# Kernel optimization log

Hardware: AMD Instinct MI355X
Metric: run time of the kernel (lower is better)

## Reference

```python
import jax, jax.numpy as jnp
import numpy as np

B, S, H, E = 32, 2048, 512, 512

def setup_inputs() -> dict:
    key = jax.random.key(0)
    ks = jax.random.split(key, 7)
    data_alpha = jax.random.normal(ks[0], (B, S, H), dtype=jnp.float32)
    data_beta  = jax.random.normal(ks[1], (B, S, H), dtype=jnp.float32)
    data_embed = jax.random.normal(ks[2], (B, S, E), dtype=jnp.float32)
    # Linear params (PyTorch-style: y = x @ W.T + b), scaled ~1/sqrt(H)
    Wb = jax.random.normal(ks[3], (E, H), dtype=jnp.float32) * (1.0 / np.sqrt(H))
    bb = jnp.zeros((E,), dtype=jnp.float32)
    Wa = jax.random.normal(ks[4], (1, H), dtype=jnp.float32) * (1.0 / np.sqrt(H))
    ba = jnp.zeros((1,), dtype=jnp.float32)
    return {"data_alpha": data_alpha, "data_beta": data_beta, "data_embed": data_embed,
            "Wb": Wb, "bb": bb, "Wa": Wa, "ba": ba}

def reference(data_alpha, data_beta, data_embed, Wb, bb, Wa, ba):
    # beta_weights = tanh(Linear(data_beta)) : [B,S,E]
    beta = jnp.tanh(jnp.einsum('bsh,eh->bse', data_beta, Wb) + bb)
    # scalar correlate per timestep, exponentiated : [B,S]
    c = jnp.einsum('bsh,oh->bso', data_alpha, Wa)[..., 0] + ba[0]
    w = jnp.exp(c)
    # Original builds alpha[b,i,j] = w[b,j]*[j<=i] / (cumsum_j<=i w) and contracts
    # sum_j alpha[b,i,j]*beta[b,j,e]*embed[b,j,e]; equivalent O(S*E) cumsum form:
    v = beta * data_embed                               # [B,S,E]
    num = jnp.cumsum(w[:, :, None] * v, axis=1)         # [B,S,E]
    den = jnp.cumsum(w, axis=1)[:, :, None] + 1e-10     # [B,S,1]
    return num / den
```

## Files before the change

kernel.cpp:

```cpp
#include <hip/hip_runtime.h>
#include <math.h>

#define Bn 32
#define Sn 2048
#define Hn 512
#define En 512
#define Mn (Bn*Sn)
#define CH 128
#define NCH (Sn/CH)
#define BK 64

using short8  = __attribute__((ext_vector_type(8))) short;
using floatx4 = __attribute__((ext_vector_type(4))) float;

__device__ __forceinline__ unsigned short f2bf(float x) {
    unsigned u = __float_as_uint(x);
    u += 0x7FFFu + ((u >> 16) & 1u);
    return (unsigned short)(u >> 16);
}

__device__ __forceinline__ float fast_tanh(float x) {
    x = fminf(20.f, fmaxf(-20.f, x));
    float e = __expf(2.f * x);
    return (e - 1.f) * __builtin_amdgcn_rcpf(e + 1.f);
}

__device__ __forceinline__ void load_lds16(const unsigned short* g, unsigned short* l) {
    __builtin_amdgcn_global_load_lds((const __attribute__((address_space(1))) void*)g,
                                     (__attribute__((address_space(3))) void*)l,
                                     16, 0, 0);
}

__global__ __launch_bounds__(256) void k_conv(const float* __restrict__ in,
                                              unsigned short* __restrict__ out, int n8) {
    int i = blockIdx.x * 256 + threadIdx.x;
    if (i >= n8) return;
    const float4 a = ((const float4*)in)[2*i];
    const float4 b = ((const float4*)in)[2*i + 1];
    short8 o;
    o[0]=f2bf(a.x); o[1]=f2bf(a.y); o[2]=f2bf(a.z); o[3]=f2bf(a.w);
    o[4]=f2bf(b.x); o[5]=f2bf(b.y); o[6]=f2bf(b.z); o[7]=f2bf(b.w);
    ((short8*)out)[i] = o;
}

__global__ __launch_bounds__(256) void k_w(const float* __restrict__ alpha,
                                           const float* __restrict__ Wa,
                                           const float* __restrict__ ba,
                                           float* __restrict__ wout) {
    const int lane = threadIdx.x & 63;
    const int wq   = threadIdx.x >> 6;
    const int row  = blockIdx.x * 4 + wq;
    const float* ap = alpha + (size_t)row * Hn + lane * 8;
    const float* wp = Wa + lane * 8;
    float4 a0 = *(const float4*)ap;
    float4 a1 = *(const float4*)(ap + 4);
    float4 w0 = *(const float4*)wp;
    float4 w1 = *(const float4*)(wp + 4);
    float s = a0.x*w0.x + a0.y*w0.y + a0.z*w0.z + a0.w*w0.w
            + a1.x*w1.x + a1.y*w1.y + a1.z*w1.z + a1.w*w1.w;
    #pragma unroll
    for (int off = 32; off; off >>= 1) s += __shfl_down(s, off, 64);
    if (lane == 0) wout[row] = expf(s + ba[0]);
}

__global__ __launch_bounds__(64) void k_scan_w(const float* __restrict__ w,
                                               float* __restrict__ cw) {
    const int b = blockIdx.x;
    const int lane = threadIdx.x;
    const float* wp = w  + (size_t)b * Sn;
    float*       cp = cw + (size_t)b * Sn;
    float carry = 0.f;
    for (int c = 0; c < Sn; c += 64) {
        float v = wp[c + lane];
        #pragma unroll
        for (int off = 1; off < 64; off <<= 1) {
            float t = __shfl_up(v, off, 64);
            if (lane >= off) v += t;
        }
        float o = carry + v;
        cp[c + lane] = o;
        carry = __shfl(o, 63, 64);
    }
}

__global__ __launch_bounds__(256) void k_gemm2(const unsigned short* __restrict__ Abf,
                                               const unsigned short* __restrict__ Bbf,
                                               const float* __restrict__ bbias,
                                               const float* __restrict__ wv,
                                               const float* __restrict__ embed,
                                               float* __restrict__ outp,
                                               float* __restrict__ partial) {
    __shared__ unsigned short lds_a[128 * BK];
    __shared__ unsigned short lds_b[128 * BK];
    const int tid  = threadIdx.x;
    const int lane = tid & 63, wq = tid >> 6;
    const int wave_n = wq & 1, wave_m = wq >> 1;
    const int blockN = blockIdx.x * 128;
    const int blockM = blockIdx.y * 128;
    const int lrow = lane & 15;
    const int quad = lane >> 4;
    const int srow = wq * 32 + (lane >> 3);
    const int scol = (lane & 7) * 8;

    floatx4 acc[4][4];
    #pragma unroll
    for (int i = 0; i < 4; i++)
        #pragma unroll
        for (int j = 0; j < 4; j++) acc[i][j] = (floatx4){0.f, 0.f, 0.f, 0.f};

    const unsigned short* Ag = Abf + (size_t)(blockM + srow) * Hn + scol;
    const unsigned short* Bg = Bbf + (size_t)(blockN + srow) * Hn + scol;
    unsigned short* la = &lds_a[(wq * 32) * BK];
    unsigned short* lb = &lds_b[(wq * 32) * BK];

    for (int k0 = 0; k0 < Hn; k0 += BK) {
        #pragma unroll
        for (int it = 0; it < 4; it++) {
            load_lds16(Ag + (size_t)(it * 8) * Hn + k0, la + it * 8 * BK);
            load_lds16(Bg + (size_t)(it * 8) * Hn + k0, lb + it * 8 * BK);
        }
        __syncthreads();
        #pragma unroll
        for (int kk = 0; kk < BK; kk += 32) {
            short8 afr[4], bfr[4];
            #pragma unroll
            for (int j = 0; j < 4; j++)
                bfr[j] = *(const short8*)&lds_b[(wave_n*64 + j*16 + lrow)*BK + kk + quad*8];
            #pragma unroll
            for (int i = 0; i < 4; i++)
                afr[i] = *(const short8*)&lds_a[(wave_m*64 + i*16 + lrow)*BK + kk + quad*8];
            #pragma unroll
            for (int i = 0; i < 4; i++)
                #pragma unroll
                for (int j = 0; j < 4; j++)
                    acc[i][j] = __builtin_amdgcn_mfma_f32_16x16x32_bf16(afr[i], bfr[j], acc[i][j], 0, 0, 0);
        }
        __syncthreads();
    }

    float colsum[4] = {0.f, 0.f, 0.f, 0.f};
    #pragma unroll
    for (int j = 0; j < 4; j++) {
        const int c = blockN + wave_n * 64 + j * 16 + lrow;
        const float bbv = bbias[c];
        #pragma unroll
        for (int i = 0; i < 4; i++) {
            const int rbase = blockM + wave_m * 64 + i * 16 + quad * 4;
            #pragma unroll
            for (int reg = 0; reg < 4; reg++) {
                const int r = rbase + reg;
                const size_t idx = (size_t)r * En + c;
                const float t = wv[r] * fast_tanh(acc[i][j][reg] + bbv) * embed[idx];
                outp[idx] = t;
                colsum[j] += t;
            }
        }
    }
    #pragma unroll
    for (int j = 0; j < 4; j++) {
        colsum[j] += __shfl_xor(colsum[j], 16, 64);
        colsum[j] += __shfl_xor(colsum[j], 32, 64);
    }
    __syncthreads();
    float* lds_f = (float*)lds_a;
    if (lane < 16) {
        #pragma unroll
        for (int j = 0; j < 4; j++) lds_f[wq * 64 + j * 16 + lane] = colsum[j];
    }
    __syncthreads();
    if (tid < 128) {
        const int wn = tid >> 6, lc = tid & 63;
        const float s = lds_f[wn * 64 + lc] + lds_f[(wn + 2) * 64 + lc];
        const int b = blockM >> 11;
        const int chunk = (blockM >> 7) & (NCH - 1);
        partial[((size_t)(b * NCH + chunk)) * En + blockN + tid] = s;
    }
}

__global__ __launch_bounds__(256) void k_cumdiv2(float* __restrict__ t,
                                                 const float* __restrict__ partial,
                                                 const float* __restrict__ cw) {
    const int eb = blockIdx.x & 1;
    const int bc = blockIdx.x >> 1;
    const int b = bc >> 4;
    const int chunk = bc & (NCH - 1);
    const int e = eb * 256 + threadIdx.x;
    float acc = 0.f;
    for (int c = 0; c < chunk; c++) acc += partial[((size_t)(b * NCH + c)) * En + e];
    const int s0 = chunk * CH;
    const float* cwp = cw + (size_t)b * Sn + s0;
    float* p = t + ((size_t)b * Sn + s0) * En + e;
    for (int s = 0; s < CH; s += 8) {
        float v[8], d[8];
        #pragma unroll
        for (int j = 0; j < 8; j++) v[j] = p[(size_t)(s + j) * En];
        #pragma unroll
        for (int j = 0; j < 8; j++) d[j] = cwp[s + j];
        #pragma unroll
        for (int j = 0; j < 8; j++) {
            acc += v[j];
            p[(size_t)(s + j) * En] = acc / (d[j] + 1e-10f);
        }
    }
}

extern "C" void kernel_launch(void* const* d_in, const int* in_sizes, int n_in,
                              void* d_out, int out_size, void* d_ws, size_t ws_size,
                              hipStream_t stream) {
    const float* alpha = (const float*)d_in[0];
    const float* beta  = (const float*)d_in[1];
    const float* embed = (const float*)d_in[2];
    const float* Wb    = (const float*)d_in[3];
    const float* bb    = (const float*)d_in[4];
    const float* Wa    = (const float*)d_in[5];
    const float* ba    = (const float*)d_in[6];
    float* out = (float*)d_out;

    unsigned short* beta_bf = (unsigned short*)d_ws;
    unsigned short* wb_bf   = beta_bf + (size_t)Mn * Hn;
    float* wbuf    = (float*)(wb_bf + (size_t)En * Hn);
    float* cwbuf   = wbuf + Mn;
    float* partial = cwbuf + Mn;

    k_conv<<<(Mn * Hn / 8 + 255) / 256, 256, 0, stream>>>(beta, beta_bf, Mn * Hn / 8);
    k_conv<<<(En * Hn / 8 + 255) / 256, 256, 0, stream>>>(Wb, wb_bf, En * Hn / 8);
    k_w<<<Mn / 4, 256, 0, stream>>>(alpha, Wa, ba, wbuf);
    k_scan_w<<<Bn, 64, 0, stream>>>(wbuf, cwbuf);
    dim3 g3(En / 128, Mn / 128);
    k_gemm2<<<g3, 256, 0, stream>>>(beta_bf, wb_bf, bb, wbuf, embed, out, partial);
    k_cumdiv2<<<Bn * NCH * 2, 256, 0, stream>>>(out, partial, cwbuf);
}
```

Measured before the change: 570.4 us.

## Fuse bf16 conversion and chunked cumsum-divide into GEMM with decoupled lookback

The separate fp32-to-bf16 conversion of data_beta is removed. The GEMM now loads fp32 A tiles into registers, converts them with packed cvt, and writes them into double-buffered, XOR-swizzled LDS. The cumulative-sum and divide pass is folded into the GEMM epilogue, using an atomic ticket ordering and chained per-chunk inclusive prefixes (status flags with spin-wait), so the intermediate output is no longer written and re-read. This removes roughly two full passes over large tensors, at the cost of serialized lookback waits across the sequence chunks and higher register and LDS pressure.

Result: slower. 973.8 us (+70.7%).

```diff
diff --git a/kernel.cpp b/kernel.cpp
--- a/kernel.cpp
+++ b/kernel.cpp
@@ -8,7 +8,11 @@
 #define Mn (Bn*Sn)
 #define CH 128
 #define NCH (Sn/CH)
+#define NBLK (En/128)
+#define NG (Bn*NBLK)
 #define BK 64
+#define NT (Hn/BK)
+#define NBLOCKS (Bn*NCH*NBLK)
 
 using short8  = __attribute__((ext_vector_type(8))) short;
 using floatx4 = __attribute__((ext_vector_type(4))) float;
@@ -17,6 +21,12 @@
     unsigned u = __float_as_uint(x);
     u += 0x7FFFu + ((u >> 16) & 1u);
     return (unsigned short)(u >> 16);
+}
+
+__device__ __forceinline__ unsigned cvt_pk_bf16(float lo, float hi) {
+    unsigned r;
+    asm("v_cvt_pk_bf16_f32 %0, %1, %2" : "=v"(r) : "v"(lo), "v"(hi));
+    return r;
 }
 
 __device__ __forceinline__ float fast_tanh(float x) {
@@ -41,6 +51,11 @@
     o[0]=f2bf(a.x); o[1]=f2bf(a.y); o[2]=f2bf(a.z); o[3]=f2bf(a.w);
     o[4]=f2bf(b.x); o[5]=f2bf(b.y); o[6]=f2bf(b.z); o[7]=f2bf(b.w);
     ((short8*)out)[i] = o;
+}
+
+__global__ __launch_bounds__(256) void k_init(unsigned* __restrict__ p, int n) {
+    int i = blockIdx.x * 256 + threadIdx.x;
+    if (i < n) p[i] = 0u;
 }
 
 __global__ __launch_bounds__(256) void k_w(const float* __restrict__ alpha,
@@ -83,24 +98,43 @@
     }
 }
 
-__global__ __launch_bounds__(256) void k_gemm2(const unsigned short* __restrict__ Abf,
-                                               const unsigned short* __restrict__ Bbf,
-                                               const float* __restrict__ bbias,
-                                               const float* __restrict__ wv,
-                                               const float* __restrict__ embed,
-                                               float* __restrict__ outp,
-                                               float* __restrict__ partial) {
-    __shared__ unsigned short lds_a[128 * BK];
-    __shared__ unsigned short lds_b[128 * BK];
+__global__ __launch_bounds__(256, 2) void k_gemm3(
+        const float* __restrict__ Af,
+        const unsigned short* __restrict__ Bbf,
+        const float* __restrict__ bbias,
+        const float* __restrict__ wv,
+        const float* __restrict__ cw,
+        const float* __restrict__ embed,
+        float* __restrict__ outp,
+        float* __restrict__ incb,
+        unsigned* __restrict__ status,
+        unsigned* __restrict__ counter)
+{
+    __shared__ char  smem[65536];
+    __shared__ float redbuf[256];
+    __shared__ float offsbuf[128];
+    __shared__ int   sticket;
+
     const int tid  = threadIdx.x;
     const int lane = tid & 63, wq = tid >> 6;
     const int wave_n = wq & 1, wave_m = wq >> 1;
-    const int blockN = blockIdx.x * 128;
-    const int blockM = blockIdx.y * 128;
-    const int lrow = lane & 15;
-    const int quad = lane >> 4;
+    const int lrow = lane & 15, quad = lane >> 4;
+
+    if (tid == 0) sticket = (int)atomicAdd(counter, 1u);
+    __syncthreads();
+    const int ticket = sticket & (NBLOCKS - 1);
+    const int cidx   = ticket >> 7;
+    const int g      = ticket & (NG - 1);
+    const int bidx   = g >> 2;
+    const int nblk   = g & (NBLK - 1);
+    const int blockM = bidx * Sn + cidx * CH;
+    const int blockN = nblk * 128;
+
     const int srow = wq * 32 + (lane >> 3);
+    const int swz8 = (lane >> 3) << 3;
     const int scol = (lane & 7) * 8;
+    const float*          Ag = Af  + (size_t)(blockM + srow) * Hn + scol;
+    const unsigned short* Bg = Bbf + (size_t)(blockN + srow) * Hn + (scol ^ swz8);
 
     floatx4 acc[4][4];
     #pragma unroll
@@ -108,98 +142,173 @@
         #pragma unroll
         for (int j = 0; j < 4; j++) acc[i][j] = (floatx4){0.f, 0.f, 0.f, 0.f};
 
-    const unsigned short* Ag = Abf + (size_t)(blockM + srow) * Hn + scol;
-    const unsigned short* Bg = Bbf + (size_t)(blockN + srow) * Hn + scol;
-    unsigned short* la = &lds_a[(wq * 32) * BK];
-    unsigned short* lb = &lds_b[(wq * 32) * BK];
-
-    for (int k0 = 0; k0 < Hn; k0 += BK) {
+    float4 areg[8];
+
+    auto loadA = [&](int k0) {
         #pragma unroll
         for (int it = 0; it < 4; it++) {
-            load_lds16(Ag + (size_t)(it * 8) * Hn + k0, la + it * 8 * BK);
+            const float* p = Ag + (size_t)(it * 8) * Hn + k0;
+            areg[2*it]     = *(const float4*)p;
+            areg[2*it + 1] = *(const float4*)(p + 4);
+        }
+    };
+    auto stageB = [&](int buf, int k0) {
+        unsigned short* lb = (unsigned short*)(smem + buf * 32768 + 16384) + (wq * 32) * BK;
+        #pragma unroll
+        for (int it = 0; it < 4; it++)
             load_lds16(Bg + (size_t)(it * 8) * Hn + k0, lb + it * 8 * BK);
-        }
-        __syncthreads();
+    };
+    auto writeA = [&](int buf) {
+        unsigned short* la = (unsigned short*)(smem + buf * 32768)
+                           + (wq * 32) * BK + ((lane * 8) ^ swz8);
+        #pragma unroll
+        for (int it = 0; it < 4; it++) {
+            const float4 a = areg[2*it], b = areg[2*it + 1];
+            uint4 o;
+            o.x = cvt_pk_bf16(a.x, a.y);
+            o.y = cvt_pk_bf16(a.z, a.w);
+            o.z = cvt_pk_bf16(b.x, b.y);
+            o.w = cvt_pk_bf16(b.z, b.w);
+            *(uint4*)(la + it * 8 * BK) = o;
+        }
+    };
+    auto compute = [&](int buf) {
+        const unsigned short* la = (const unsigned short*)(smem + buf * 32768);
+        const unsigned short* lb = (const unsigned short*)(smem + buf * 32768 + 16384);
+        const int swzr = (lrow & 7) << 3;
         #pragma unroll
         for (int kk = 0; kk < BK; kk += 32) {
             short8 afr[4], bfr[4];
             #pragma unroll
             for (int j = 0; j < 4; j++)
-                bfr[j] = *(const short8*)&lds_b[(wave_n*64 + j*16 + lrow)*BK + kk + quad*8];
+                bfr[j] = *(const short8*)&lb[(wave_n*64 + j*16 + lrow)*BK + ((kk + quad*8) ^ swzr)];
             #pragma unroll
             for (int i = 0; i < 4; i++)
-                afr[i] = *(const short8*)&lds_a[(wave_m*64 + i*16 + lrow)*BK + kk + quad*8];
+                afr[i] = *(const short8*)&la[(wave_m*64 + i*16 + lrow)*BK + ((kk + quad*8) ^ swzr)];
             #pragma unroll
             for (int i = 0; i < 4; i++)
                 #pragma unroll
                 for (int j = 0; j < 4; j++)
                     acc[i][j] = __builtin_amdgcn_mfma_f32_16x16x32_bf16(afr[i], bfr[j], acc[i][j], 0, 0, 0);
         }
+    };
+
+    loadA(0);
+    stageB(0, 0);
+    writeA(0);
+    __syncthreads();
+    #pragma unroll
+    for (int t = 0; t < NT - 1; ++t) {
+        const int cur = t & 1;
+        loadA((t + 1) * BK);
+        stageB(cur ^ 1, (t + 1) * BK);
+        compute(cur);
+        writeA(cur ^ 1);
         __syncthreads();
     }
-
-    float colsum[4] = {0.f, 0.f, 0.f, 0.f};
+    compute((NT - 1) & 1);
+
+    const float* wvp = wv + blockM;
+    const float* cwp = cw + blockM;
+    float wr[4][4];
+    #pragma unroll
+    for (int i = 0; i < 4; i++)
+        #pragma unroll
+        for (int reg = 0; reg < 4; reg++)
+            wr[i][reg] = wvp[wave_m*64 + i*16 + quad*4 + reg];
+
     #pragma unroll
     for (int j = 0; j < 4; j++) {
-        const int c = blockN + wave_n * 64 + j * 16 + lrow;
+        const int c = blockN + wave_n*64 + j*16 + lrow;
         const float bbv = bbias[c];
         #pragma unroll
         for (int i = 0; i < 4; i++) {
-            const int rbase = blockM + wave_m * 64 + i * 16 + quad * 4;
-            #pragma unroll
-            for (int reg = 0; reg < 4; reg++) {
-                const int r = rbase + reg;
-                const size_t idx = (size_t)r * En + c;
-                const float t = wv[r] * fast_tanh(acc[i][j][reg] + bbv) * embed[idx];
-                outp[idx] = t;
-                colsum[j] += t;
-            }
-        }
-    }
+            const int rl = wave_m*64 + i*16 + quad*4;
+            const float* ep = embed + (size_t)(blockM + rl) * En + c;
+            #pragma unroll
+            for (int reg = 0; reg < 4; reg++)
+                acc[i][j][reg] = wr[i][reg] * fast_tanh(acc[i][j][reg] + bbv)
+                               * ep[(size_t)reg * En];
+        }
+    }
+
+    float colsum[4];
     #pragma unroll
     for (int j = 0; j < 4; j++) {
-        colsum[j] += __shfl_xor(colsum[j], 16, 64);
-        colsum[j] += __shfl_xor(colsum[j], 32, 64);
+        float s = 0.f;
+        #pragma unroll
+        for (int i = 0; i < 4; i++)
+            #pragma unroll
+            for (int reg = 0; reg < 4; reg++) s += acc[i][j][reg];
+        s += __shfl_xor(s, 16, 64);
+        s += __shfl_xor(s, 32, 64);
+        colsum[j] = s;
+    }
+    if (lane < 16) {
+        #pragma unroll
+        for (int j = 0; j < 4; j++) redbuf[wq*64 + j*16 + lane] = colsum[j];
     }
     __syncthreads();
-    float* lds_f = (float*)lds_a;
-    if (lane < 16) {
-        #pragma unroll
-        for (int j = 0; j < 4; j++) lds_f[wq * 64 + j * 16 + lane] = colsum[j];
-    }
+
+    const int sidx = g * NCH + cidx;
+    float* myinc = incb + (size_t)sidx * 128;
+    if (cidx > 0) {
+        if (tid == 0) {
+            while (__hip_atomic_load(&status[sidx - 1], __ATOMIC_ACQUIRE,
+                                     __HIP_MEMORY_SCOPE_AGENT) == 0u)
+                __builtin_amdgcn_s_sleep(2);
+        }
+        __syncthreads();
+    }
+    if (tid < 128) {
+        float off = 0.f;
+        if (cidx > 0)
+            off = __hip_atomic_load(incb + (size_t)(sidx - 1) * 128 + tid,
+                                    __ATOMIC_RELAXED, __HIP_MEMORY_SCOPE_AGENT);
+        offsbuf[tid] = off;
+        const float tot = redbuf[tid] + redbuf[128 + tid];
+        __hip_atomic_store(myinc + tid, off + tot,
+                           __ATOMIC_RELAXED, __HIP_MEMORY_SCOPE_AGENT);
+    }
+    __threadfence();
     __syncthreads();
-    if (tid < 128) {
-        const int wn = tid >> 6, lc = tid & 63;
-        const float s = lds_f[wn * 64 + lc] + lds_f[(wn + 2) * 64 + lc];
-        const int b = blockM >> 11;
-        const int chunk = (blockM >> 7) & (NCH - 1);
-        partial[((size_t)(b * NCH + chunk)) * En + blockN + tid] = s;
-    }
-}
-
-__global__ __launch_bounds__(256) void k_cumdiv2(float* __restrict__ t,
-                                                 const float* __restrict__ partial,
-                                                 const float* __restrict__ cw) {
-    const int eb = blockIdx.x & 1;
-    const int bc = blockIdx.x >> 1;
-    const int b = bc >> 4;
-    const int chunk = bc & (NCH - 1);
-    const int e = eb * 256 + threadIdx.x;
-    float acc = 0.f;
-    for (int c = 0; c < chunk; c++) acc += partial[((size_t)(b * NCH + c)) * En + e];
-    const int s0 = chunk * CH;
-    const float* cwp = cw + (size_t)b * Sn + s0;
-    float* p = t + ((size_t)b * Sn + s0) * En + e;
-    for (int s = 0; s < CH; s += 8) {
-        float v[8], d[8];
-        #pragma unroll
-        for (int j = 0; j < 8; j++) v[j] = p[(size_t)(s + j) * En];
-        #pragma unroll
-        for (int j = 0; j < 8; j++) d[j] = cwp[s + j];
-        #pragma unroll
-        for (int j = 0; j < 8; j++) {
-            acc += v[j];
-            p[(size_t)(s + j) * En] = acc / (d[j] + 1e-10f);
+    if (tid == 0)
+        __hip_atomic_store(&status[sidx], 1u, __ATOMIC_RELEASE, __HIP_MEMORY_SCOPE_AGENT);
+
+    float drcp[4][4];
+    #pragma unroll
+    for (int i = 0; i < 4; i++)
+        #pragma unroll
+        for (int reg = 0; reg < 4; reg++)
+            drcp[i][reg] = __builtin_amdgcn_rcpf(
+                cwp[wave_m*64 + i*16 + quad*4 + reg] + 1e-10f);
+
+    #pragma unroll
+    for (int j = 0; j < 4; j++) {
+        const int colh = wave_n*64 + j*16 + lrow;
+        const int c = blockN + colh;
+        float base = offsbuf[colh];
+        if (wave_m) base += redbuf[colh];
+        #pragma unroll
+        for (int i = 0; i < 4; i++) {
+            const float p0 = acc[i][j][0];
+            const float p1 = p0 + acc[i][j][1];
+            const float p2 = p1 + acc[i][j][2];
+            const float p3 = p2 + acc[i][j][3];
+            float x = p3;
+            float u = __shfl_up(x, 16, 64);
+            if (quad >= 1) x += u;
+            u = __shfl_up(x, 32, 64);
+            if (quad >= 2) x += u;
+            const float excl = x - p3;
+            const float itot = __shfl(x, 48 + lrow, 64);
+            const int rl = wave_m*64 + i*16 + quad*4;
+            float* op = outp + (size_t)(blockM + rl) * En + c;
+            op[0]              = (base + excl + p0) * drcp[i][0];
+            op[(size_t)En]     = (base + excl + p1) * drcp[i][1];
+            op[(size_t)2*En]   = (base + excl + p2) * drcp[i][2];
+            op[(size_t)3*En]   = (base + excl + p3) * drcp[i][3];
+            base += itot;
         }
     }
 }
@@ -216,17 +325,17 @@
     const float* ba    = (const float*)d_in[6];
     float* out = (float*)d_out;
 
-    unsigned short* beta_bf = (unsigned short*)d_ws;
-    unsigned short* wb_bf   = beta_bf + (size_t)Mn * Hn;
-    float* wbuf    = (float*)(wb_bf + (size_t)En * Hn);
-    float* cwbuf   = wbuf + Mn;
-    float* partial = cwbuf + Mn;
-
-    k_conv<<<(Mn * Hn / 8 + 255) / 256, 256, 0, stream>>>(beta, beta_bf, Mn * Hn / 8);
+    unsigned short* wb_bf = (unsigned short*)d_ws;
+    float* wbuf     = (float*)(wb_bf + (size_t)En * Hn);
+    float* cwbuf    = wbuf + Mn;
+    float* incb     = cwbuf + Mn;
+    unsigned* status  = (unsigned*)(incb + (size_t)NG * NCH * 128);
+    unsigned* counter = status + NG * NCH;
+
+    k_init<<<(NG * NCH + 1 + 255) / 256, 256, 0, stream>>>(status, NG * NCH + 1);
     k_conv<<<(En * Hn / 8 + 255) / 256, 256, 0, stream>>>(Wb, wb_bf, En * Hn / 8);
     k_w<<<Mn / 4, 256, 0, stream>>>(alpha, Wa, ba, wbuf);
     k_scan_w<<<Bn, 64, 0, stream>>>(wbuf, cwbuf);
-    dim3 g3(En / 128, Mn / 128);
-    k_gemm2<<<g3, 256, 0, stream>>>(beta_bf, wb_bf, bb, wbuf, embed, out, partial);
-    k_cumdiv2<<<Bn * NCH * 2, 256, 0, stream>>>(out, partial, cwbuf);
-}
+    k_gemm3<<<NBLOCKS, 256, 0, stream>>>(beta, wb_bf, bb, wbuf, cwbuf, embed,
+                                         out, incb, status, counter);
+}
```
